# Kernel tuning notes

Measured on AMD Instinct MI355X. Metric: run time of the kernel, lower is better.

## Reference

```python
import jax, jax.numpy as jnp
import numpy as np
import math

D_MODEL = 1024
N_HEAD = 16
D_K = D_MODEL // N_HEAD
B, S = 2, 2048


def setup_inputs() -> dict:
    key = jax.random.key(0)
    ks = jax.random.split(key, 9)
    sc = 0.02
    return {
        "x": jax.random.normal(ks[0], (B, S, D_MODEL), dtype=jnp.float32),
        "Wq": jax.random.normal(ks[1], (D_MODEL, D_MODEL), dtype=jnp.float32) * sc,
        "bq": jnp.zeros((D_MODEL,), dtype=jnp.float32),
        "Wk": jax.random.normal(ks[2], (D_MODEL, D_MODEL), dtype=jnp.float32) * sc,
        "bk": jnp.zeros((D_MODEL,), dtype=jnp.float32),
        "Wv": jax.random.normal(ks[3], (D_MODEL, D_MODEL), dtype=jnp.float32) * sc,
        "bv": jnp.zeros((D_MODEL,), dtype=jnp.float32),
        "Wo": jax.random.normal(ks[4], (D_MODEL, D_MODEL), dtype=jnp.float32) * sc,
        "bo": jnp.zeros((D_MODEL,), dtype=jnp.float32),
    }


def reference(x, Wq, bq, Wk, bk, Wv, bv, Wo, bo):
    # cache=None prefill path: q_start=0, k_len=S (S <= MAX_CACHE_LEN)
    b, s, d = x.shape
    # projections (torch Linear: x @ W.T + b)
    q = (x @ Wq.T + bq).reshape(b, s, N_HEAD, D_K).transpose(0, 2, 1, 3)  # [b,h,s,dk]
    k = (x @ Wk.T + bk).reshape(b, s, N_HEAD, D_K).transpose(0, 2, 1, 3)
    v = (x @ Wv.T + bv).reshape(b, s, N_HEAD, D_K).transpose(0, 2, 1, 3)
    scores = jnp.einsum("bhqd,bhkd->bhqk", q, k) / math.sqrt(D_K)
    causal = jnp.triu(jnp.ones((s, s), dtype=bool), k=1)  # True above diagonal
    scores = jnp.where(causal[None, None], -jnp.inf, scores)
    attn = jax.nn.softmax(scores, axis=-1)  # dropout p=0 (eval)
    ctx = jnp.einsum("bhqk,bhkd->bhqd", attn, v)
    ctx = ctx.transpose(0, 2, 1, 3).reshape(b, s, d)
    return ctx @ Wo.T + bo
```

## Files before the change

kernel.cpp:

```cpp
#include <hip/hip_runtime.h>
#include <hip/hip_bf16.h>

#define DM 1024
#define NH 16
#define DK 64
#define BB 2
#define SS 2048
#define NTOK (BB*SS)
#define SCALE_LOG2E 0.1803368801111204f

typedef __attribute__((ext_vector_type(8))) short bf16x8;
typedef __attribute__((ext_vector_type(4))) short s16x4;
typedef __attribute__((ext_vector_type(4))) float f32x4;
typedef __attribute__((ext_vector_type(4))) unsigned short us4;

#define GLOAD16(gp, lp) \
  __builtin_amdgcn_global_load_lds((const __attribute__((address_space(1))) void*)(gp), \
                                   (__attribute__((address_space(3))) void*)(lp), 16, 0, 0)

__device__ inline unsigned short f2b(float f) {
  unsigned int x = __float_as_uint(f);
  return (unsigned short)((x + 0x7FFFu + ((x >> 16) & 1u)) >> 16);
}
__device__ inline unsigned int pack2bf(float a, float b) {
  unsigned int r;
  asm("v_cvt_pk_bf16_f32 %0, %1, %2" : "=v"(r) : "v"(a), "v"(b));
  return r;
}

__device__ inline f32x4 mfma16(s16x4 a, s16x4 b, f32x4 c) {
#if __has_builtin(__builtin_amdgcn_mfma_f32_16x16x16bf16_1k)
  return __builtin_amdgcn_mfma_f32_16x16x16bf16_1k(a, b, c, 0, 0, 0);
#else
  f32x4 d;
  asm("v_mfma_f32_16x16x16_bf16 %0, %1, %2, %3"
      : "=v"(d) : "v"(a), "v"(b), "0"(c));
  return d;
#endif
}

#define XC4 (NTOK*DM/4)
#define WC4 (DM*DM/4)
__global__ void cast_all(const float* __restrict__ x,  const float* __restrict__ wq,
                         const float* __restrict__ wk, const float* __restrict__ wv,
                         const float* __restrict__ wo,
                         unsigned short* __restrict__ xb,  unsigned short* __restrict__ wqb,
                         unsigned short* __restrict__ wkb, unsigned short* __restrict__ wvb,
                         unsigned short* __restrict__ wob) {
  const int total = XC4 + 4*WC4;
  int i = blockIdx.x * blockDim.x + threadIdx.x;
  int stride = gridDim.x * blockDim.x;
  for (; i < total; i += stride) {
    const float* s; unsigned short* d; int off;
    if (i < XC4) { s = x; d = xb; off = i; }
    else {
      int j = i - XC4;
      int sel = j >> 18;
      off = j & (WC4 - 1);
      if      (sel == 0) { s = wq; d = wqb; }
      else if (sel == 1) { s = wk; d = wkb; }
      else if (sel == 2) { s = wv; d = wvb; }
      else               { s = wo; d = wob; }
    }
    float4 v = reinterpret_cast<const float4*>(s)[off];
    us4 o;
    o[0] = f2b(v.x); o[1] = f2b(v.y); o[2] = f2b(v.z); o[3] = f2b(v.w);
    reinterpret_cast<us4*>(d)[off] = o;
  }
}

__device__ __forceinline__ void gemm_mainloop(const unsigned short* __restrict__ A,
                                              const unsigned short* __restrict__ W,
                                              unsigned short* As, unsigned short* Bs,
                                              int m0, int n0, int tid, f32x4 acc[4][2]) {
  const int lane = tid & 63;
  const int w = tid >> 6;
  const int wr = w >> 1, wc = w & 1;
  const int g = lane >> 4, q = lane & 15;

  const int col0 = (((lane & 7) ^ ((lane >> 3) & 7)) << 3);
  const unsigned short* Ag = A + (size_t)(m0 + w*32 + (lane >> 3)) * DM + col0;
  const unsigned short* Bg = W + (size_t)(n0 + w*16 + (lane >> 3)) * DM + col0;
  char* AsB = (char*)As + w * 4096;
  char* BsB = (char*)Bs + w * 2048;

  const int fso = ((g ^ (q & 7)) << 4);

  for (int kt = 0; kt < DM; kt += 64) {
    __syncthreads();
    GLOAD16(Ag + kt,          AsB);
    GLOAD16(Ag + kt +  8*DM,  AsB + 1024);
    GLOAD16(Ag + kt + 16*DM,  AsB + 2048);
    GLOAD16(Ag + kt + 24*DM,  AsB + 3072);
    GLOAD16(Bg + kt,          BsB);
    GLOAD16(Bg + kt +  8*DM,  BsB + 1024);
    __syncthreads();
    #pragma unroll
    for (int h = 0; h < 2; h++) {
      const int so = fso ^ (h << 6);
      bf16x8 aF[4], bF[2];
      #pragma unroll
      for (int mt = 0; mt < 4; mt++)
        aF[mt] = *reinterpret_cast<const bf16x8*>((char*)As + (wr*64 + mt*16 + q)*128 + so);
      #pragma unroll
      for (int nt = 0; nt < 2; nt++)
        bF[nt] = *reinterpret_cast<const bf16x8*>((char*)Bs + (wc*32 + nt*16 + q)*128 + so);
      #pragma unroll
      for (int mt = 0; mt < 4; mt++)
        #pragma unroll
        for (int nt = 0; nt < 2; nt++)
          acc[mt][nt] = __builtin_amdgcn_mfma_f32_16x16x32_bf16(aF[mt], bF[nt], acc[mt][nt], 0, 0, 0);
    }
  }
}

__global__ __launch_bounds__(256, 2)
void gemm_qkv(const unsigned short* __restrict__ xb,
              const unsigned short* __restrict__ wqb, const unsigned short* __restrict__ wkb,
              const unsigned short* __restrict__ wvb,
              const float* __restrict__ bq, const float* __restrict__ bk,
              const float* __restrict__ bv,
              unsigned short* __restrict__ qo, unsigned short* __restrict__ ko,
              unsigned short* __restrict__ vto) {
  __shared__ unsigned short As[128*64];
  __shared__ unsigned short Bs[64*64];
  const int z = blockIdx.z;
  const unsigned short* W = (z == 0) ? wqb : (z == 1) ? wkb : wvb;
  const float* bias = (z == 0) ? bq : (z == 1) ? bk : bv;
  const int m0 = blockIdx.y * 128, n0 = blockIdx.x * 64;

  f32x4 acc[4][2];
  #pragma unroll
  for (int i = 0; i < 4; i++)
    #pragma unroll
    for (int j = 0; j < 2; j++)
      #pragma unroll
      for (int e = 0; e < 4; e++) acc[i][j][e] = 0.f;

  gemm_mainloop(xb, W, As, Bs, m0, n0, threadIdx.x, acc);

  const int lane = threadIdx.x & 63, w = threadIdx.x >> 6;
  const int wr = w >> 1, wc = w & 1, g = lane >> 4, q = lane & 15;
  const float sc = (z == 0) ? SCALE_LOG2E : 1.0f;
  #pragma unroll
  for (int mt = 0; mt < 4; mt++) {
    #pragma unroll
    for (int nt = 0; nt < 2; nt++) {
      const int mg0 = m0 + wr*64 + mt*16 + 4*g;
      const int ng  = n0 + wc*32 + nt*16 + q;
      const float bv_ = bias[ng];
      const int h = ng >> 6, d = ng & 63;
      if (z == 2) {
        const int b = mg0 >> 11, s = mg0 & 2047;
        us4 pk;
        #pragma unroll
        for (int r = 0; r < 4; r++) pk[r] = f2b(acc[mt][nt][r] + bv_);
        *reinterpret_cast<us4*>(&vto[((size_t)((b*NH + h)*DK + d)) * SS + s]) = pk;
      } else {
        unsigned short* out = (z == 0) ? qo : ko;
        #pragma unroll
        for (int r = 0; r < 4; r++) {
          const int m = mg0 + r;
          const int b = m >> 11, s = m & 2047;
          out[((size_t)((b*NH + h)*SS + s)) * DK + d] = f2b((acc[mt][nt][r] + bv_) * sc);
        }
      }
    }
  }
}

__global__ __launch_bounds__(256, 2)
void gemm_out(const unsigned short* __restrict__ ctx,
              const unsigned short* __restrict__ wob,
              const float* __restrict__ bo, float* __restrict__ out) {
  __shared__ unsigned short As[128*64];
  __shared__ unsigned short Bs[64*64];
  const int m0 = blockIdx.y * 128, n0 = blockIdx.x * 64;
  f32x4 acc[4][2];
  #pragma unroll
  for (int i = 0; i < 4; i++)
    #pragma unroll
    for (int j = 0; j < 2; j++)
      #pragma unroll
      for (int e = 0; e < 4; e++) acc[i][j][e] = 0.f;

  gemm_mainloop(ctx, wob, As, Bs, m0, n0, threadIdx.x, acc);

  const int lane = threadIdx.x & 63, w = threadIdx.x >> 6;
  const int wr = w >> 1, wc = w & 1, g = lane >> 4, q = lane & 15;
  #pragma unroll
  for (int mt = 0; mt < 4; mt++) {
    #pragma unroll
    for (int nt = 0; nt < 2; nt++) {
      const int mg0 = m0 + wr*64 + mt*16 + 4*g;
      const int ng  = n0 + wc*32 + nt*16 + q;
      const float bv_ = bo[ng];
      #pragma unroll
      for (int r = 0; r < 4; r++)
        out[(size_t)(mg0 + r) * DM + ng] = acc[mt][nt][r] + bv_;
    }
  }
}

__global__ __launch_bounds__(256, 2)
void attn_fwd(const unsigned short* __restrict__ Q,
              const unsigned short* __restrict__ Kg,
              const unsigned short* __restrict__ VT,
              unsigned short* __restrict__ ctx) {
  __shared__ float CMB[2][64][66];
  __shared__ float CML[2][64];
  const int qblk = (int)gridDim.y - 1 - (int)blockIdx.y;
  const int bh = blockIdx.x;
  const int tid = threadIdx.x;
  const int lane = tid & 63;
  const int w = tid >> 6;
  const int g = lane >> 4;
  const int q = lane & 15;
  const int q0 = qblk * 64;
  const int T = qblk + 1;
  const size_t base = (size_t)bh * SS * DK;

  bf16x8 aQ[4][2];
  #pragma unroll
  for (int rg = 0; rg < 4; rg++) {
    const unsigned short* qp = Q + base + (size_t)(q0 + rg*16 + q) * DK + g*8;
    aQ[rg][0] = *reinterpret_cast<const bf16x8*>(qp);
    aQ[rg][1] = *reinterpret_cast<const bf16x8*>(qp + 32);
  }

  f32x4 o[4][4];
  float l_run[4];
  #pragma unroll
  for (int rg = 0; rg < 4; rg++) {
    #pragma unroll
    for (int dt = 0; dt < 4; dt++)
      #pragma unroll
      for (int r = 0; r < 4; r++) o[rg][dt][r] = 0.f;
    l_run[rg] = 0.f;
  }

  bf16x8 aK[4][2];
  s16x4 aV16[4][4];
  if (w < T) {
    #pragma unroll
    for (int f = 0; f < 4; f++) {
      const unsigned short* kp = Kg + base + (size_t)(w*64 + f*16 + q) * DK + g*8;
      aK[f][0] = *reinterpret_cast<const bf16x8*>(kp);
      aK[f][1] = *reinterpret_cast<const bf16x8*>(kp + 32);
    }
    #pragma unroll
    for (int dt = 0; dt < 4; dt++)
      #pragma unroll
      for (int f = 0; f < 4; f++)
        aV16[dt][f] = *reinterpret_cast<const s16x4*>(
            VT + base + (size_t)(dt*16 + q) * SS + w*64 + f*16 + 4*g);
  }

  for (int t = w; t < T; t += 4) {
    const bool tail = (t == T - 1);
    #pragma unroll
    for (int rg = 0; rg < 4; rg++) {
      f32x4 sf[4];
      __builtin_amdgcn_s_setprio(1);
      #pragma unroll
      for (int f = 0; f < 4; f++) {
        f32x4 z;
        #pragma unroll
        for (int r = 0; r < 4; r++) z[r] = 0.f;
        z = __builtin_amdgcn_mfma_f32_16x16x32_bf16(aK[f][0], aQ[rg][0], z, 0, 0, 0);
        z = __builtin_amdgcn_mfma_f32_16x16x32_bf16(aK[f][1], aQ[rg][1], z, 0, 0, 0);
        sf[f] = z;
      }
      __builtin_amdgcn_s_setprio(0);

      if (rg == 3 && t + 4 < T) {
        #pragma unroll
        for (int f = 0; f < 4; f++) {
          const unsigned short* kp = Kg + base + (size_t)((t+4)*64 + f*16 + q) * DK + g*8;
          aK[f][0] = *reinterpret_cast<const bf16x8*>(kp);
          aK[f][1] = *reinterpret_cast<const bf16x8*>(kp + 32);
        }
      }

      const int grow = q0 + rg*16 + q;
      float p[4][4];
      float ps = 0.f;
      #pragma unroll
      for (int f = 0; f < 4; f++)
        #pragma unroll
        for (int r = 0; r < 4; r++) {
          float v = sf[f][r];
          if (tail) {
            int gcol = t*64 + f*16 + 4*g + r;
            if (gcol > grow) v = -1e30f;
          }
          float e = exp2f(v);
          p[f][r] = e;
          ps += e;
        }
      ps += __shfl_xor(ps, 16);
      ps += __shfl_xor(ps, 32);
      l_run[rg] += ps;

      s16x4 pb[4];
      #pragma unroll
      for (int f = 0; f < 4; f++) {
        unsigned int lo = pack2bf(p[f][0], p[f][1]);
        unsigned int hi = pack2bf(p[f][2], p[f][3]);
        pb[f][0] = (short)(lo & 0xFFFF);
        pb[f][1] = (short)(lo >> 16);
        pb[f][2] = (short)(hi & 0xFFFF);
        pb[f][3] = (short)(hi >> 16);
      }

      __builtin_amdgcn_s_setprio(1);
      #pragma unroll
      for (int f = 0; f < 4; f++)
        #pragma unroll
        for (int dt = 0; dt < 4; dt++)
          o[rg][dt] = mfma16(aV16[dt][f], pb[f], o[rg][dt]);
      __builtin_amdgcn_s_setprio(0);
    }

    if (t + 4 < T) {
      #pragma unroll
      for (int dt = 0; dt < 4; dt++)
        #pragma unroll
        for (int f = 0; f < 4; f++)
          aV16[dt][f] = *reinterpret_cast<const s16x4*>(
              VT + base + (size_t)(dt*16 + q) * SS + (t+4)*64 + f*16 + 4*g);
    }
  }

  if (w >= 2) {
    const int slot = w - 2;
    #pragma unroll
    for (int rg = 0; rg < 4; rg++) {
      #pragma unroll
      for (int dt = 0; dt < 4; dt++)
        #pragma unroll
        for (int r = 0; r < 4; r++)
          CMB[slot][rg*16 + q][dt*16 + 4*g + r] = o[rg][dt][r];
      CML[slot][rg*16 + q] = l_run[rg];
    }
  }
  __syncthreads();
  if (w < 2) {
    const int slot = w;
    #pragma unroll
    for (int rg = 0; rg < 4; rg++) {
      l_run[rg] += CML[slot][rg*16 + q];
      #pragma unroll
      for (int dt = 0; dt < 4; dt++)
        #pragma unroll
        for (int r = 0; r < 4; r++)
          o[rg][dt][r] += CMB[slot][rg*16 + q][dt*16 + 4*g + r];
    }
  }
  __syncthreads();
  if (w == 1) {
    #pragma unroll
    for (int rg = 0; rg < 4; rg++) {
      #pragma unroll
      for (int dt = 0; dt < 4; dt++)
        #pragma unroll
        for (int r = 0; r < 4; r++)
          CMB[0][rg*16 + q][dt*16 + 4*g + r] = o[rg][dt][r];
      CML[0][rg*16 + q] = l_run[rg];
    }
  }
  __syncthreads();
  if (w == 0) {
    const int b = bh >> 4, h = bh & 15;
    #pragma unroll
    for (int rg = 0; rg < 4; rg++) {
      float lfin = l_run[rg] + CML[0][rg*16 + q];
      const float inv = 1.0f / lfin;
      const int s = q0 + rg*16 + q;
      #pragma unroll
      for (int dt = 0; dt < 4; dt++) {
        us4 pkv;
        #pragma unroll
        for (int r = 0; r < 4; r++) {
          float val = o[rg][dt][r] + CMB[0][rg*16 + q][dt*16 + 4*g + r];
          pkv[r] = f2b(val * inv);
        }
        *reinterpret_cast<us4*>(&ctx[((size_t)(b*SS + s)) * DM + h*DK + dt*16 + 4*g]) = pkv;
      }
    }
  }
}

extern "C" void kernel_launch(void* const* d_in, const int* in_sizes, int n_in,
                              void* d_out, int out_size, void* d_ws, size_t ws_size,
                              hipStream_t stream) {
  const float* x  = (const float*)d_in[0];
  const float* Wq = (const float*)d_in[1];
  const float* bq = (const float*)d_in[2];
  const float* Wk = (const float*)d_in[3];
  const float* bk = (const float*)d_in[4];
  const float* Wv = (const float*)d_in[5];
  const float* bv = (const float*)d_in[6];
  const float* Wo = (const float*)d_in[7];
  const float* bo = (const float*)d_in[8];
  float* out = (float*)d_out;

  unsigned short* xb  = (unsigned short*)d_ws;
  unsigned short* wqb = xb  + (size_t)NTOK * DM;
  unsigned short* wkb = wqb + (size_t)DM * DM;
  unsigned short* wvb = wkb + (size_t)DM * DM;
  unsigned short* wob = wvb + (size_t)DM * DM;
  unsigned short* q   = wob + (size_t)DM * DM;
  unsigned short* k   = q   + (size_t)NTOK * DM;
  unsigned short* vt  = k   + (size_t)NTOK * DM;
  unsigned short* ctx = vt  + (size_t)NTOK * DM;

  cast_all<<<2048, 256, 0, stream>>>(x, Wq, Wk, Wv, Wo, xb, wqb, wkb, wvb, wob);

  gemm_qkv<<<dim3(DM/64, NTOK/128, 3), 256, 0, stream>>>(xb, wqb, wkb, wvb,
                                                         bq, bk, bv, q, k, vt);

  attn_fwd<<<dim3(BB*NH, SS/64), 256, 0, stream>>>(q, k, vt, ctx);

  gemm_out<<<dim3(DM/64, NTOK/128), 256, 0, stream>>>(ctx, wob, bo, out);
}
```

Baseline: 126.9 us.

## Double-buffer K registers, load V per tile, use native exp2, defer rowsum

Restructures the attention inner loop so K fragments for tile t+4 are prefetched into an alternate register buffer (kA/kB ping-pong) at the start of each tile instead of midway, and V is loaded at the start of each tile with 16-byte loads that are then split into halves by lane. exp2f is replaced with the hardware v_exp_f32 builtin, and the row-sum reduction is moved after the PV MFMAs so the shuffles can overlap matrix work. The intent is to hide global load latency and trim VALU cost in the softmax, at the cost of more live registers, which may reduce occupancy or cause spills. V is no longer prefetched a tile ahead, so its load latency is now exposed just before use.

```diff
diff --git a/kernel.cpp b/kernel.cpp
--- a/kernel.cpp
+++ b/kernel.cpp
@@ -27,7 +27,15 @@
   asm("v_cvt_pk_bf16_f32 %0, %1, %2" : "=v"(r) : "v"(a), "v"(b));
   return r;
 }
-
+__device__ inline float exp2v(float x) {
+#if __has_builtin(__builtin_amdgcn_exp2f)
+  return __builtin_amdgcn_exp2f(x);
+#else
+  float r;
+  asm("v_exp_f32 %0, %1" : "=v"(r) : "v"(x));
+  return r;
+#endif
+}
 __device__ inline f32x4 mfma16(s16x4 a, s16x4 b, f32x4 c) {
 #if __has_builtin(__builtin_amdgcn_mfma_f32_16x16x16bf16_1k)
   return __builtin_amdgcn_mfma_f32_16x16x16bf16_1k(a, b, c, 0, 0, 0);
@@ -219,6 +227,7 @@
   const int q0 = qblk * 64;
   const int T = qblk + 1;
   const size_t base = (size_t)bh * SS * DK;
+  const bool ghalf = (g & 1);
 
   bf16x8 aQ[4][2];
   #pragma unroll
@@ -239,98 +248,111 @@
     l_run[rg] = 0.f;
   }
 
-  bf16x8 aK[4][2];
-  s16x4 aV16[4][4];
+  bf16x8 kA[4][2], kB[4][2];
+  s16x4 av[4][4];
+
+  #define LOADK(kk, t) do { \
+    _Pragma("unroll") \
+    for (int f = 0; f < 4; f++) { \
+      const unsigned short* kp = Kg + base + (size_t)((t)*64 + f*16 + q) * DK + g*8; \
+      kk[f][0] = *reinterpret_cast<const bf16x8*>(kp); \
+      kk[f][1] = *reinterpret_cast<const bf16x8*>(kp + 32); \
+    } \
+  } while (0)
+
+  #define LOADV(t) do { \
+    _Pragma("unroll") \
+    for (int dt = 0; dt < 4; dt++) { \
+      _Pragma("unroll") \
+      for (int f = 0; f < 4; f++) { \
+        bf16x8 vf = *reinterpret_cast<const bf16x8*>( \
+            VT + base + (size_t)(dt*16 + q) * SS + (t)*64 + f*16 + (g >> 1)*8); \
+        s16x4 lo_ = {vf[0], vf[1], vf[2], vf[3]}; \
+        s16x4 hi_ = {vf[4], vf[5], vf[6], vf[7]}; \
+        av[dt][f] = ghalf ? hi_ : lo_; \
+      } \
+    } \
+  } while (0)
+
+  #define COMPUTE(t, kk) do { \
+    const bool tail = ((t) == T - 1); \
+    _Pragma("unroll") \
+    for (int rg = 0; rg < 4; rg++) { \
+      f32x4 sf[4]; \
+      __builtin_amdgcn_s_setprio(1); \
+      _Pragma("unroll") \
+      for (int f = 0; f < 4; f++) { \
+        f32x4 z; \
+        _Pragma("unroll") \
+        for (int r = 0; r < 4; r++) z[r] = 0.f; \
+        z = __builtin_amdgcn_mfma_f32_16x16x32_bf16(kk[f][0], aQ[rg][0], z, 0, 0, 0); \
+        z = __builtin_amdgcn_mfma_f32_16x16x32_bf16(kk[f][1], aQ[rg][1], z, 0, 0, 0); \
+        sf[f] = z; \
+      } \
+      __builtin_amdgcn_s_setprio(0); \
+      const int grow = q0 + rg*16 + q; \
+      float p[4][4]; \
+      _Pragma("unroll") \
+      for (int f = 0; f < 4; f++) { \
+        _Pragma("unroll") \
+        for (int r = 0; r < 4; r++) { \
+          float v = sf[f][r]; \
+          if (tail) { \
+            int gcol = (t)*64 + f*16 + 4*g + r; \
+            if (gcol > grow) v = -1e30f; \
+          } \
+          p[f][r] = exp2v(v); \
+        } \
+      } \
+      s16x4 pb[4]; \
+      _Pragma("unroll") \
+      for (int f = 0; f < 4; f++) { \
+        unsigned int lo = pack2bf(p[f][0], p[f][1]); \
+        unsigned int hi = pack2bf(p[f][2], p[f][3]); \
+        pb[f][0] = (short)(lo & 0xFFFF); \
+        pb[f][1] = (short)(lo >> 16); \
+        pb[f][2] = (short)(hi & 0xFFFF); \
+        pb[f][3] = (short)(hi >> 16); \
+      } \
+      __builtin_amdgcn_s_setprio(1); \
+      _Pragma("unroll") \
+      for (int f = 0; f < 4; f++) { \
+        _Pragma("unroll") \
+        for (int dt = 0; dt < 4; dt++) \
+          o[rg][dt] = mfma16(av[dt][f], pb[f], o[rg][dt]); \
+      } \
+      __builtin_amdgcn_s_setprio(0); \
+      float ps = 0.f; \
+      _Pragma("unroll") \
+      for (int f = 0; f < 4; f++) { \
+        _Pragma("unroll") \
+        for (int r = 0; r < 4; r++) ps += p[f][r]; \
+      } \
+      ps += __shfl_xor(ps, 16); \
+      ps += __shfl_xor(ps, 32); \
+      l_run[rg] += ps; \
+    } \
+  } while (0)
+
   if (w < T) {
-    #pragma unroll
-    for (int f = 0; f < 4; f++) {
-      const unsigned short* kp = Kg + base + (size_t)(w*64 + f*16 + q) * DK + g*8;
-      aK[f][0] = *reinterpret_cast<const bf16x8*>(kp);
-      aK[f][1] = *reinterpret_cast<const bf16x8*>(kp + 32);
-    }
-    #pragma unroll
-    for (int dt = 0; dt < 4; dt++)
-      #pragma unroll
-      for (int f = 0; f < 4; f++)
-        aV16[dt][f] = *reinterpret_cast<const s16x4*>(
-            VT + base + (size_t)(dt*16 + q) * SS + w*64 + f*16 + 4*g);
-  }
-
-  for (int t = w; t < T; t += 4) {
-    const bool tail = (t == T - 1);
-    #pragma unroll
-    for (int rg = 0; rg < 4; rg++) {
-      f32x4 sf[4];
-      __builtin_amdgcn_s_setprio(1);
-      #pragma unroll
-      for (int f = 0; f < 4; f++) {
-        f32x4 z;
-        #pragma unroll
-        for (int r = 0; r < 4; r++) z[r] = 0.f;
-        z = __builtin_amdgcn_mfma_f32_16x16x32_bf16(aK[f][0], aQ[rg][0], z, 0, 0, 0);
-        z = __builtin_amdgcn_mfma_f32_16x16x32_bf16(aK[f][1], aQ[rg][1], z, 0, 0, 0);
-        sf[f] = z;
-      }
-      __builtin_amdgcn_s_setprio(0);
-
-      if (rg == 3 && t + 4 < T) {
-        #pragma unroll
-        for (int f = 0; f < 4; f++) {
-          const unsigned short* kp = Kg + base + (size_t)((t+4)*64 + f*16 + q) * DK + g*8;
-          aK[f][0] = *reinterpret_cast<const bf16x8*>(kp);
-          aK[f][1] = *reinterpret_cast<const bf16x8*>(kp + 32);
-        }
-      }
-
-      const int grow = q0 + rg*16 + q;
-      float p[4][4];
-      float ps = 0.f;
-      #pragma unroll
-      for (int f = 0; f < 4; f++)
-        #pragma unroll
-        for (int r = 0; r < 4; r++) {
-          float v = sf[f][r];
-          if (tail) {
-            int gcol = t*64 + f*16 + 4*g + r;
-            if (gcol > grow) v = -1e30f;
-          }
-          float e = exp2f(v);
-          p[f][r] = e;
-          ps += e;
-        }
-      ps += __shfl_xor(ps, 16);
-      ps += __shfl_xor(ps, 32);
-      l_run[rg] += ps;
-
-      s16x4 pb[4];
-      #pragma unroll
-      for (int f = 0; f < 4; f++) {
-        unsigned int lo = pack2bf(p[f][0], p[f][1]);
-        unsigned int hi = pack2bf(p[f][2], p[f][3]);
-        pb[f][0] = (short)(lo & 0xFFFF);
-        pb[f][1] = (short)(lo >> 16);
-        pb[f][2] = (short)(hi & 0xFFFF);
-        pb[f][3] = (short)(hi >> 16);
-      }
-
-      __builtin_amdgcn_s_setprio(1);
-      #pragma unroll
-      for (int f = 0; f < 4; f++)
-        #pragma unroll
-        for (int dt = 0; dt < 4; dt++)
-          o[rg][dt] = mfma16(aV16[dt][f], pb[f], o[rg][dt]);
-      __builtin_amdgcn_s_setprio(0);
-    }
-
-    if (t + 4 < T) {
-      #pragma unroll
-      for (int dt = 0; dt < 4; dt++)
-        #pragma unroll
-        for (int f = 0; f < 4; f++)
-          aV16[dt][f] = *reinterpret_cast<const s16x4*>(
-              VT + base + (size_t)(dt*16 + q) * SS + (t+4)*64 + f*16 + 4*g);
-    }
-  }
+    LOADK(kA, w);
+    int t = w;
+    while (true) {
+      LOADV(t);
+      if (t + 4 < T) LOADK(kB, t + 4);
+      COMPUTE(t, kA);
+      t += 4;
+      if (t >= T) break;
+      LOADV(t);
+      if (t + 4 < T) LOADK(kA, t + 4);
+      COMPUTE(t, kB);
+      t += 4;
+      if (t >= T) break;
+    }
+  }
+  #undef LOADK
+  #undef LOADV
+  #undef COMPUTE
 
   if (w >= 2) {
     const int slot = w - 2;
```

Result: slower. 197.6 us (+55.7%).
